# Performance work log

Measured on AMD Instinct MI355X. Metric: run time of the kernel, lower is better.

The kernel has to match this reference:

```python
import jax, jax.numpy as jnp
import numpy as np

H = 64  # base_hidden_size
SIGMA = 0.1
TAU = 1.0
T1 = 5
T2 = 5
NEG = 1e10


def setup_inputs() -> dict:
    key = jax.random.key(0)
    ks = jax.random.split(key, 24)
    B = 16
    R = 8
    n_cities = 1023
    n_nodes = n_cities + 1  # 1024

    x_a_state = jax.random.uniform(ks[0], (B, R, n_nodes), dtype=jnp.float32)
    assignment_prev = jnp.zeros((B, R, n_nodes), dtype=jnp.float32)
    # action: one-hot-ish; each robot picks a node. Use zeros + set robot r -> node r (valid: presence all ones)
    action = jnp.zeros((B, R, n_nodes), dtype=jnp.float32)
    action = action.at[:, jnp.arange(R), jnp.arange(R)].set(1.0)
    edge = jax.random.uniform(ks[1], (B, n_cities, n_nodes, 3), dtype=jnp.float32)
    avail_node_presence = jnp.ones((B, 1, n_nodes), dtype=jnp.float32)
    avail_robot = jnp.ones((B, 1, R), dtype=jnp.float32)

    def lin(k, i, o):
        # torch Linear weight [o, i]; store transposed [i, o]
        bound = 1.0 / np.sqrt(i)
        return jax.random.uniform(k, (i, o), dtype=jnp.float32, minval=-bound, maxval=bound)

    params = {
        'W1_presence': lin(ks[2], 3, H),
        'W2_presence': lin(ks[3], H, 1),
        'W_x_1a': lin(ks[4], 1, H),
        'W_emb_1a': lin(ks[5], 1, H),
        'W_l_1a': lin(ks[6], H, H),
        'W_x_1b': lin(ks[7], 1, H),
        'W_emb_1b': lin(ks[8], 1, H),
        'W_l_1b': lin(ks[9], H, H),
        'W_x_2': lin(ks[10], 2 * H, 2 * H),
        'W_emb_2': lin(ks[11], 1, 2 * H),
        'W_l_2': lin(ks[12], 2 * H, 2 * H),
        'W_Q': lin(ks[13], 2 * H, 1),
    }

    # noise initial states (randn in torch forward; make them explicit inputs for determinism)
    u_a0 = SIGMA * jax.random.normal(ks[14], (B, n_nodes, H), dtype=jnp.float32)
    u_b0 = SIGMA * jax.random.normal(ks[15], (B, n_nodes, H), dtype=jnp.float32)
    gamma0 = SIGMA * jax.random.normal(ks[16], (B, n_nodes, 2 * H), dtype=jnp.float32)

    return dict(x_a_state=x_a_state, assignment_prev=assignment_prev, action=action,
                edge=edge, avail_node_presence=avail_node_presence,
                u_a0=u_a0, u_b0=u_b0, gamma0=gamma0, **params)


def reference(x_a_state, assignment_prev, action, edge, avail_node_presence,
              u_a0, u_b0, gamma0,
              W1_presence, W2_presence, W_x_1a, W_emb_1a, W_l_1a,
              W_x_1b, W_emb_1b, W_l_1b, W_x_2, W_emb_2, W_l_2, W_Q):
    B, n_cities, n_nodes, _ = edge.shape

    assignment = assignment_prev + action  # [B,R,N]
    x_a = jnp.max(x_a_state * assignment, axis=1, keepdims=True)  # [B,1,N]
    x_a = jnp.transpose(x_a, (0, 2, 1))  # [B,N,1]

    # presence attention
    h1 = jax.nn.relu(edge @ W1_presence)          # [B,C,N,H]
    h2 = jax.nn.relu(h1 @ W2_presence)[..., 0]    # [B,C,N]
    h2 = h2 / TAU
    eye = jnp.eye(n_cities, n_nodes, dtype=edge.dtype)
    mask = (1.0 - eye)[None] * avail_node_presence  # [B,C,N]
    logit = h2 * mask - (1.0 - mask) * NEG
    presence_out = jax.nn.softmax(logit, axis=-1)   # [B,C,N]
    presence_in = jnp.transpose(presence_out, (0, 2, 1))  # [B,N,C]

    edge_dist = jnp.transpose(edge[:, :, :, 0:1], (0, 2, 1, 3))  # [B,N,C,1]

    # T1 loop (faithful to original incl. the l_a reuse in u_b update)
    emb_1a = jax.nn.sigmoid(edge_dist @ W_emb_1a)  # [B,N,C,H]
    emb_1b = jax.nn.sigmoid(edge_dist @ W_emb_1b)  # computed each iter but constant
    x_a_1a = x_a @ W_x_1a  # [B,N,H]
    x_a_1b = x_a @ W_x_1b

    u_a = u_a0
    for _ in range(T1):
        # u_a[:, :-1, :] gathered per target node i, weighted by emb and presence_in
        # l_a[b,i,h] = sum_c presence_in[b,i,c] * u_a[b,c,h] * emb_1a[b,i,c,h]
        l_a = jnp.einsum('bic,bch,bich->bih', presence_in, u_a[:, :-1, :], emb_1a)
        u_a = jax.nn.relu(l_a @ W_l_1a + x_a_1a)
        u_b = jax.nn.relu(l_a @ W_l_1b + x_a_1b)  # original uses l_a (bug kept)
    u_concat = jnp.concatenate([u_a, u_b], axis=-1)  # [B,N,2H]

    emb_2 = jax.nn.sigmoid(edge_dist @ W_emb_2)  # [B,N,C,2H]
    x2 = u_concat @ W_x_2  # [B,N,2H]
    gamma = gamma0
    for _ in range(T2):
        l_2 = jnp.einsum('bic,bch,bich->bih', presence_in, gamma[:, :-1, :], emb_2)
        gamma = jax.nn.relu(l_2 @ W_l_2 + x2)

    Q_utility = gamma @ W_Q  # [B,N,1]
    Q = jnp.sum(Q_utility, axis=1)  # [B,1]
    return Q
```

## Files before the change

kernel.cpp:

```cpp
#include <hip/hip_runtime.h>

#define BATCH 16
#define RB    8
#define CITIES 1023
#define NODES 1024
#define HDIM  64
#define H2DIM 128
#define KTOT  3072

#define C1f 0.24944119f
#define C3f (-0.01850586f)

typedef __bf16    bf16x8 __attribute__((ext_vector_type(8)));
typedef _Float16  f16x8  __attribute__((ext_vector_type(8)));
typedef _Float16  f16x2  __attribute__((ext_vector_type(2)));
typedef float     f32x4  __attribute__((ext_vector_type(4)));

__device__ __forceinline__ f32x4 mfma16(bf16x8 a, bf16x8 b, f32x4 c){
    return __builtin_amdgcn_mfma_f32_16x16x32_bf16(a, b, c, 0, 0, 0);
}
__device__ __forceinline__ f32x4 mfma16h(f16x8 a, f16x8 b, f32x4 c){
    return __builtin_amdgcn_mfma_f32_16x16x32_f16(a, b, c, 0, 0, 0);
}
__device__ __forceinline__ unsigned short f2b(float f){
    __bf16 b = (__bf16)f;
    return __builtin_bit_cast(unsigned short, b);
}
__device__ __forceinline__ float b2f(unsigned short u){
    unsigned int t = ((unsigned int)u) << 16;
    return __builtin_bit_cast(float, t);
}
__device__ __forceinline__ unsigned short f2h(float f){
    _Float16 h = (_Float16)f;
    return __builtin_bit_cast(unsigned short, h);
}
__device__ __forceinline__ float h2f(unsigned short u){
    return (float)__builtin_bit_cast(_Float16, u);
}
__device__ __forceinline__ void async16(const void* g, void* l){
    __builtin_amdgcn_global_load_lds(
        (const __attribute__((address_space(1))) unsigned int*)g,
        (__attribute__((address_space(3))) unsigned int*)l, 16, 0, 0);
}
template<int N>
__device__ __forceinline__ void wait_vmcnt(){
    asm volatile("s_waitcnt vmcnt(%0)" :: "i"(N) : "memory");
}

__global__ __launch_bounds__(256) void xa_k(const float* __restrict__ xs,
        const float* __restrict__ ap, const float* __restrict__ act,
        float* __restrict__ xa){
    int idx = blockIdx.x*256 + threadIdx.x;
    int b = idx >> 10, n = idx & 1023;
    float m = -1e30f;
    #pragma unroll
    for(int r=0;r<RB;r++){
        size_t o = (((size_t)b*RB + r)<<10) + n;
        m = fmaxf(m, xs[o]*(ap[o]+act[o]));
    }
    xa[idx] = m;
}

__global__ __launch_bounds__(128) void presence_k(const float* __restrict__ edge,
        const float* __restrict__ W1, const float* __restrict__ W2,
        const float* __restrict__ avail,
        unsigned short* __restrict__ P, unsigned short* __restrict__ D){
    int c = blockIdx.x, b = blockIdx.y;
    int tid = threadIdx.x;
    __shared__ f16x8 Wpk[32];
    __shared__ float red[2];
    if(tid < 32){
        int h0 = tid*2;
        f16x8 w;
        w[0]=(_Float16)W1[h0];       w[1]=(_Float16)W1[h0+1];
        w[2]=(_Float16)W1[64+h0];    w[3]=(_Float16)W1[64+h0+1];
        w[4]=(_Float16)W1[128+h0];   w[5]=(_Float16)W1[128+h0+1];
        w[6]=(_Float16)W2[h0];       w[7]=(_Float16)W2[h0+1];
        Wpk[tid] = w;
    }
    __syncthreads();
    f16x2 e0d[8], e1d[8], e2d[8];
    float acc[8];
    size_t ebase = (((size_t)b*CITIES + c)<<10)*3;
    #pragma unroll
    for(int j=0;j<8;j++){
        int n = tid + j*128;
        size_t ea = ebase + (size_t)n*3;
        _Float16 v0=(_Float16)edge[ea], v1=(_Float16)edge[ea+1], v2=(_Float16)edge[ea+2];
        e0d[j]=(f16x2){v0,v0}; e1d[j]=(f16x2){v1,v1}; e2d[j]=(f16x2){v2,v2};
        acc[j]=0.f;
    }
    const f16x2 z2 = {(_Float16)0, (_Float16)0};
    for(int hp=0;hp<32;hp++){
        f16x8 w = Wpk[hp];
        f16x2 wx={w[0],w[1]}, wy={w[2],w[3]}, wz={w[4],w[5]}, w2={w[6],w[7]};
        #pragma unroll
        for(int j=0;j<8;j++){
            f16x2 a = e0d[j]*wx + e1d[j]*wy + e2d[j]*wz;
            a = __builtin_elementwise_max(a, z2);
            acc[j] = __builtin_amdgcn_fdot2(a, w2, acc[j], false);
        }
    }
    float lg[8], ex[8];
    #pragma unroll
    for(int j=0;j<8;j++){
        int n = tid + j*128;
        float h2 = fmaxf(acc[j], 0.f);
        float mk = (n==c) ? 0.f : avail[(b<<10)+n];
        lg[j] = h2*mk - (1.f-mk)*1e10f;
    }
    int wv = tid>>6, ln = tid&63;
    float mx = -1e30f;
    #pragma unroll
    for(int j=0;j<8;j++) mx = fmaxf(mx, lg[j]);
    for(int o=32;o>0;o>>=1) mx = fmaxf(mx, __shfl_xor(mx,o,64));
    if(ln==0) red[wv]=mx;
    __syncthreads();
    mx = fmaxf(red[0],red[1]);
    __syncthreads();
    float s = 0.f;
    #pragma unroll
    for(int j=0;j<8;j++){ ex[j] = expf(lg[j]-mx); s += ex[j]; }
    for(int o=32;o>0;o>>=1) s += __shfl_xor(s,o,64);
    if(ln==0) red[wv]=s;
    __syncthreads();
    s = red[0]+red[1];
    float inv = 1.f/s;
    size_t pbase = ((size_t)b*CITIES + c)<<10;
    #pragma unroll
    for(int j=0;j<8;j++){
        int n = tid + j*128;
        P[pbase+n] = f2h(ex[j]*inv);
        D[pbase+n] = __builtin_bit_cast(unsigned short, e0d[j][0]);
    }
}

__global__ __launch_bounds__(256) void abuild_k(const unsigned short* __restrict__ P,
        const unsigned short* __restrict__ D, unsigned short* __restrict__ A){
    int ct = blockIdx.x, nt = blockIdx.y, b = blockIdx.z;
    int tid = threadIdx.x;
    __shared__ unsigned short Pt[32][36];
    __shared__ unsigned short Dt[32][36];
    {
        int crow = tid>>3, ng = (tid&7)<<2;
        int c = ct*32 + crow;
        if(c < CITIES){
            size_t o = (((size_t)b*CITIES + c)<<10) + nt*32 + ng;
            *(ushort4*)&Pt[crow][ng] = *(const ushort4*)&P[o];
            *(ushort4*)&Dt[crow][ng] = *(const ushort4*)&D[o];
        } else {
            ushort4 z; z.x=0;z.y=0;z.z=0;z.w=0;
            *(ushort4*)&Pt[crow][ng] = z;
            *(ushort4*)&Dt[crow][ng] = z;
        }
    }
    __syncthreads();
    int nrow = tid>>3, cg = (tid&7)<<2;
    ushort4 w0, w1, w2;
    #pragma unroll
    for(int j=0;j<4;j++){
        float p = h2f(Pt[cg+j][nrow]);
        float d = h2f(Dt[cg+j][nrow]);
        float d3 = d*d*d;
        ((unsigned short*)&w0)[j] = f2h(p);
        ((unsigned short*)&w1)[j] = f2h(p*d);
        ((unsigned short*)&w2)[j] = f2h(p*d3);
    }
    size_t abase = ((size_t)(b<<10) + nt*32 + nrow)*KTOT + ct*32 + cg;
    *(ushort4*)&A[abase]      = w0;
    *(ushort4*)&A[abase+1024] = w1;
    *(ushort4*)&A[abase+2048] = w2;
}

__global__ __launch_bounds__(256) void binit_k(const float* __restrict__ U0,
        const float* __restrict__ We, unsigned short* __restrict__ BT, int nout){
    int kc = blockIdx.x*256 + threadIdx.x;
    int h = blockIdx.y, b = blockIdx.z;
    int k = kc >> 10, c = kc & 1023;
    float we = We[h];
    float q = (k==0) ? 0.5f : (k==1 ? C1f*we : C3f*we*we*we);
    float u = (c < CITIES) ? U0[(((size_t)b<<10) + c)*nout + h] : 0.f;
    BT[((size_t)(b*nout + h))*KTOT + kc] = f2h(q*u);
}

#define SR 72

template<bool LAST>
__global__ __launch_bounds__(256) void fused1_k(const unsigned short* __restrict__ Ap,
        const unsigned short* __restrict__ BT,
        const float* __restrict__ Wl1a, const float* __restrict__ Wl1b,
        const float* __restrict__ Wx1a, const float* __restrict__ Wx1b,
        const float* __restrict__ We1a, const float* __restrict__ xa,
        unsigned short* __restrict__ Bnext, float* __restrict__ ua, float* __restrict__ ub){
    int mt = blockIdx.x, b = blockIdx.y;
    int i0 = mt*64;
    int tid = threadIdx.x, wave=tid>>6, lane=tid&63, quad=lane>>4, l16=lane&15;
    __shared__ __align__(16) char smem[49152];
    unsigned short* Lh = (unsigned short*)smem;
    unsigned short* Ll = (unsigned short*)(smem + 9216);
    unsigned short* Wh = (unsigned short*)(smem + 18432);
    unsigned short* Wo = (unsigned short*)(smem + 27648);

    f32x4 zero = {0.f,0.f,0.f,0.f};
    f32x4 gacc[4] = {zero,zero,zero,zero};
    const unsigned short* pa[2];
    const unsigned short* pb[2];
    #pragma unroll
    for(int rd=0; rd<2; rd++){
        int idx = rd*256 + tid, r = idx>>3, ch = idx&7;
        pa[rd] = Ap + ((size_t)(b<<10) + i0 + r)*KTOT + ((ch ^ (r&7))<<3);
        pb[rd] = BT + ((size_t)b*64 + r)*KTOT + ((ch ^ (r&7))<<3);
    }
    int sw = l16&7;
    auto stage = [&](char* buf){
        unsigned short* At = (unsigned short*)buf;
        unsigned short* Bt = At + 4096;
        #pragma unroll
        for(int rd=0; rd<2; rd++){ async16(pa[rd], At + rd*2048 + tid*8); pa[rd] += 64; }
        #pragma unroll
        for(int rd=0; rd<2; rd++){ async16(pb[rd], Bt + rd*2048 + tid*8); pb[rd] += 64; }
    };
    auto comp = [&](const char* buf){
        const unsigned short* At = (const unsigned short*)buf;
        const unsigned short* Bt = At + 4096;
        #pragma unroll
        for(int kb=0; kb<2; kb++){
            f16x8 af = *(const f16x8*)&At[(wave*16 + l16)*64 + (((kb*4+quad)^sw)<<3)];
            #pragma unroll
            for(int nt=0; nt<4; nt++){
                f16x8 bf = *(const f16x8*)&Bt[(nt*16 + l16)*64 + (((kb*4+quad)^sw)<<3)];
                gacc[nt] = mfma16h(af, bf, gacc[nt]);
            }
        }
    };
    char* b0 = smem; char* b1 = smem + 16384; char* b2 = smem + 32768;
    stage(b0); stage(b1);
    wait_vmcnt<4>(); __builtin_amdgcn_s_barrier();
    for(int kk=0; kk<46; kk++){
        stage(b2);
        comp(b0);
        wait_vmcnt<4>(); __builtin_amdgcn_s_barrier();
        char* tp=b0; b0=b1; b1=b2; b2=tp;
    }
    comp(b0);
    wait_vmcnt<0>(); __builtin_amdgcn_s_barrier();
    comp(b1);
    __syncthreads();
    #pragma unroll
    for(int nt=0; nt<4; nt++){
        int h = nt*16 + l16;
        #pragma unroll
        for(int rr=0; rr<4; rr++){
            int i = wave*16 + quad*4 + rr;
            float v = gacc[nt][rr];
            unsigned short hh = f2b(v);
            Lh[i*SR + h] = hh;
            Ll[i*SR + h] = f2b(v - b2f(hh));
        }
    }
    {
        int k = tid>>2, n0 = (tid&3)*16;
        for(int j=0;j<16;j++){
            float w = Wl1a[k*64 + n0 + j];
            unsigned short hh = f2b(w);
            Wh[(n0+j)*SR + k] = hh;
            Wo[(n0+j)*SR + k] = f2b(w - b2f(hh));
        }
    }
    __syncthreads();
    f32x4 acc[4] = {zero,zero,zero,zero};
    #pragma unroll
    for(int kc=0;kc<2;kc++){
        bf16x8 ah = *(const bf16x8*)&Lh[(wave*16+l16)*SR + kc*32 + quad*8];
        bf16x8 al = *(const bf16x8*)&Ll[(wave*16+l16)*SR + kc*32 + quad*8];
        #pragma unroll
        for(int nt=0;nt<4;nt++){
            bf16x8 bh = *(const bf16x8*)&Wh[(nt*16+l16)*SR + kc*32 + quad*8];
            bf16x8 bl = *(const bf16x8*)&Wo[(nt*16+l16)*SR + kc*32 + quad*8];
            acc[nt] = mfma16(ah, bh, acc[nt]);
            acc[nt] = mfma16(ah, bl, acc[nt]);
            acc[nt] = mfma16(al, bh, acc[nt]);
        }
    }
    int gi = i0 + wave*16 + quad*4;
    float4 xav = *(const float4*)&xa[(b<<10) + gi];
    float xr[4] = {xav.x, xav.y, xav.z, xav.w};
    if(!LAST){
        #pragma unroll
        for(int nt=0;nt<4;nt++){
            int h = nt*16 + l16;
            float wx = Wx1a[h];
            float we = We1a[h];
            float q1 = C1f*we, q2 = C3f*we*we*we;
            ushort4 w0,w1,w2;
            #pragma unroll
            for(int rr=0;rr<4;rr++){
                float u = fmaxf(acc[nt][rr] + xr[rr]*wx, 0.f);
                bool pad = (gi+rr == 1023);
                ((unsigned short*)&w0)[rr] = pad?(unsigned short)0:f2h(0.5f*u);
                ((unsigned short*)&w1)[rr] = pad?(unsigned short)0:f2h(q1*u);
                ((unsigned short*)&w2)[rr] = pad?(unsigned short)0:f2h(q2*u);
            }
            size_t base = ((size_t)(b*64 + h))*KTOT + gi;
            *(ushort4*)&Bnext[base]      = w0;
            *(ushort4*)&Bnext[base+1024] = w1;
            *(ushort4*)&Bnext[base+2048] = w2;
        }
    } else {
        #pragma unroll
        for(int nt=0;nt<4;nt++){
            int h = nt*16+l16; float wx = Wx1a[h];
            #pragma unroll
            for(int rr=0;rr<4;rr++)
                ua[(((size_t)b<<10)+gi+rr)*64 + h] = fmaxf(acc[nt][rr] + xr[rr]*wx, 0.f);
        }
        __syncthreads();
        { int k = tid>>2, n0 = (tid&3)*16;
          for(int j=0;j<16;j++){
              float w = Wl1b[k*64 + n0 + j];
              unsigned short hh = f2b(w);
              Wh[(n0+j)*SR + k] = hh;
              Wo[(n0+j)*SR + k] = f2b(w - b2f(hh));
          } }
        __syncthreads();
        f32x4 acc2[4] = {zero,zero,zero,zero};
        #pragma unroll
        for(int kc=0;kc<2;kc++){
            bf16x8 ah = *(const bf16x8*)&Lh[(wave*16+l16)*SR + kc*32 + quad*8];
            bf16x8 al = *(const bf16x8*)&Ll[(wave*16+l16)*SR + kc*32 + quad*8];
            #pragma unroll
            for(int nt=0;nt<4;nt++){
                bf16x8 bh = *(const bf16x8*)&Wh[(nt*16+l16)*SR + kc*32 + quad*8];
                bf16x8 bl = *(const bf16x8*)&Wo[(nt*16+l16)*SR + kc*32 + quad*8];
                acc2[nt] = mfma16(ah, bh, acc2[nt]);
                acc2[nt] = mfma16(ah, bl, acc2[nt]);
                acc2[nt] = mfma16(al, bh, acc2[nt]);
            }
        }
        #pragma unroll
        for(int nt=0;nt<4;nt++){
            int h = nt*16+l16; float wx = Wx1b[h];
            #pragma unroll
            for(int rr=0;rr<4;rr++)
                ub[(((size_t)b<<10)+gi+rr)*64 + h] = fmaxf(acc2[nt][rr] + xr[rr]*wx, 0.f);
        }
    }
}

__global__ __launch_bounds__(256) void x2_k(const float* __restrict__ ua,
        const float* __restrict__ ub, const float* __restrict__ Wx2,
        float* __restrict__ x2){
    int mt = blockIdx.x, b = blockIdx.y;
    int i0 = mt*64;
    int tid = threadIdx.x, wave=tid>>6, lane=tid&63, quad=lane>>4, l16=lane&15;
    __shared__ __align__(16) unsigned short Uh[64*SR], Ul[64*SR];
    __shared__ __align__(16) unsigned short Wh[128*SR], Wo[128*SR];
    f32x4 zero = {0.f,0.f,0.f,0.f};
    f32x4 acc[8];
    #pragma unroll
    for(int nt=0;nt<8;nt++) acc[nt]=zero;
    for(int ph=0; ph<2; ph++){
        if(ph) __syncthreads();
        {
            int k = tid>>2, n0 = (tid&3)*32;
            for(int j=0;j<32;j++){
                float w = Wx2[(ph*64 + k)*128 + n0 + j];
                unsigned short hh = f2b(w);
                Wh[(n0+j)*SR + k] = hh;
                Wo[(n0+j)*SR + k] = f2b(w - b2f(hh));
            }
            int i = tid>>2, c0 = (tid&3)*16;
            const float* src = (ph ? ub : ua) + (((size_t)b<<10)+i0+i)*64 + c0;
            #pragma unroll
            for(int j=0;j<4;j++){
                float4 v = *(const float4*)(src + j*4);
                float vv[4] = {v.x, v.y, v.z, v.w};
                #pragma unroll
                for(int t=0;t<4;t++){
                    unsigned short hh = f2b(vv[t]);
                    Uh[i*SR + c0 + j*4 + t] = hh;
                    Ul[i*SR + c0 + j*4 + t] = f2b(vv[t] - b2f(hh));
                }
            }
        }
        __syncthreads();
        #pragma unroll
        for(int kc=0;kc<2;kc++){
            bf16x8 ah = *(const bf16x8*)&Uh[(wave*16+l16)*SR + kc*32 + quad*8];
            bf16x8 al = *(const bf16x8*)&Ul[(wave*16+l16)*SR + kc*32 + quad*8];
            #pragma unroll
            for(int nt=0;nt<8;nt++){
                bf16x8 bh = *(const bf16x8*)&Wh[(nt*16+l16)*SR + kc*32 + quad*8];
                bf16x8 bl = *(const bf16x8*)&Wo[(nt*16+l16)*SR + kc*32 + quad*8];
                acc[nt] = mfma16(ah, bh, acc[nt]);
                acc[nt] = mfma16(ah, bl, acc[nt]);
                acc[nt] = mfma16(al, bh, acc[nt]);
            }
        }
    }
    int gi = i0 + wave*16 + quad*4;
    #pragma unroll
    for(int nt=0;nt<8;nt++){
        int h = nt*16 + l16;
        #pragma unroll
        for(int rr=0;rr<4;rr++)
            x2[(((size_t)b<<10)+gi+rr)*128 + h] = acc[nt][rr];
    }
}

template<bool LAST>
__global__ __launch_bounds__(256) void fused2_k(const unsigned short* __restrict__ Ap,
        const unsigned short* __restrict__ BT,
        const float* __restrict__ Wl2, const float* __restrict__ x2,
        const float* __restrict__ We2, const float* __restrict__ WQ,
        unsigned short* __restrict__ Bnext, float* __restrict__ out){
    int mt = blockIdx.x, b = blockIdx.y;
    int i0 = mt*64;
    int tid = threadIdx.x, wave=tid>>6, lane=tid&63, quad=lane>>4, l16=lane&15;
    extern __shared__ __align__(16) char smem[];
    __shared__ float red[4];
    unsigned short* Lh = (unsigned short*)smem;
    unsigned short* Ll = (unsigned short*)(smem + 9216);
    unsigned short* Wh = (unsigned short*)(smem + 18432);
    unsigned short* Wo = (unsigned short*)(smem + 36864);

    f32x4 zero = {0.f,0.f,0.f,0.f};
    f32x4 gacc[8] = {zero,zero,zero,zero,zero,zero,zero,zero};
    const unsigned short* pa[2];
    const unsigned short* pb[4];
    #pragma unroll
    for(int rd=0; rd<2; rd++){
        int idx = rd*256 + tid, r = idx>>3, ch = idx&7;
        pa[rd] = Ap + ((size_t)(b<<10) + i0 + r)*KTOT + ((ch ^ (r&7))<<3);
    }
    #pragma unroll
    for(int rd=0; rd<4; rd++){
        int idx = rd*256 + tid, r = idx>>3, ch = idx&7;
        pb[rd] = BT + ((size_t)b*128 + r)*KTOT + ((ch ^ (r&7))<<3);
    }
    int sw = l16&7;
    auto stage = [&](char* buf){
        unsigned short* At = (unsigned short*)buf;
        unsigned short* Bt = At + 4096;
        #pragma unroll
        for(int rd=0; rd<2; rd++){ async16(pa[rd], At + rd*2048 + tid*8); pa[rd] += 64; }
        #pragma unroll
        for(int rd=0; rd<4; rd++){ async16(pb[rd], Bt + rd*2048 + tid*8); pb[rd] += 64; }
    };
    auto comp = [&](const char* buf){
        const unsigned short* At = (const unsigned short*)buf;
        const unsigned short* Bt = At + 4096;
        #pragma unroll
        for(int kb=0; kb<2; kb++){
            f16x8 af = *(const f16x8*)&At[(wave*16 + l16)*64 + (((kb*4+quad)^sw)<<3)];
            #pragma unroll
            for(int nt=0; nt<8; nt++){
                f16x8 bf = *(const f16x8*)&Bt[(nt*16 + l16)*64 + (((kb*4+quad)^sw)<<3)];
                gacc[nt] = mfma16h(af, bf, gacc[nt]);
            }
        }
    };
    char* b0 = smem; char* b1 = smem + 24576; char* b2 = smem + 49152;
    stage(b0); stage(b1);
    wait_vmcnt<6>(); __builtin_amdgcn_s_barrier();
    for(int kk=0; kk<46; kk++){
        stage(b2);
        comp(b0);
        wait_vmcnt<6>(); __builtin_amdgcn_s_barrier();
        char* tp=b0; b0=b1; b1=b2; b2=tp;
    }
    comp(b0);
    wait_vmcnt<0>(); __builtin_amdgcn_s_barrier();
    comp(b1);
    __syncthreads();
    f32x4 fac[8] = {zero,zero,zero,zero,zero,zero,zero,zero};
    #pragma unroll
    for(int ph=0; ph<2; ph++){
        if(ph) __syncthreads();
        #pragma unroll
        for(int ntl=0; ntl<4; ntl++){
            int h = ntl*16 + l16;
            #pragma unroll
            for(int rr=0; rr<4; rr++){
                int i = wave*16 + quad*4 + rr;
                float v = gacc[ph*4 + ntl][rr];
                unsigned short hh = f2b(v);
                Lh[i*SR + h] = hh;
                Ll[i*SR + h] = f2b(v - b2f(hh));
            }
        }
        {
            int k = tid>>2, n0 = (tid&3)*32;
            for(int j=0;j<32;j++){
                float w = Wl2[(ph*64 + k)*128 + n0 + j];
                unsigned short hh = f2b(w);
                Wh[(n0+j)*SR + k] = hh;
                Wo[(n0+j)*SR + k] = f2b(w - b2f(hh));
            }
        }
        __syncthreads();
        #pragma unroll
        for(int kc=0;kc<2;kc++){
            bf16x8 ah = *(const bf16x8*)&Lh[(wave*16+l16)*SR + kc*32 + quad*8];
            bf16x8 al = *(const bf16x8*)&Ll[(wave*16+l16)*SR + kc*32 + quad*8];
            #pragma unroll
            for(int nt=0;nt<8;nt++){
                bf16x8 bh = *(const bf16x8*)&Wh[(nt*16+l16)*SR + kc*32 + quad*8];
                bf16x8 bl = *(const bf16x8*)&Wo[(nt*16+l16)*SR + kc*32 + quad*8];
                fac[nt] = mfma16(ah, bh, fac[nt]);
                fac[nt] = mfma16(ah, bl, fac[nt]);
                fac[nt] = mfma16(al, bh, fac[nt]);
            }
        }
    }
    int gi = i0 + wave*16 + quad*4;
    float qp = 0.f;
    #pragma unroll
    for(int nt=0;nt<8;nt++){
        int h = nt*16 + l16;
        float g[4];
        #pragma unroll
        for(int rr=0;rr<4;rr++)
            g[rr] = fmaxf(fac[nt][rr] + x2[(((size_t)b<<10)+gi+rr)*128 + h], 0.f);
        if(!LAST){
            float we = We2[h];
            float q1 = C1f*we, q2 = C3f*we*we*we;
            ushort4 w0,w1,w2;
            #pragma unroll
            for(int rr=0;rr<4;rr++){
                bool pad = (gi+rr == 1023);
                ((unsigned short*)&w0)[rr] = pad?(unsigned short)0:f2h(0.5f*g[rr]);
                ((unsigned short*)&w1)[rr] = pad?(unsigned short)0:f2h(q1*g[rr]);
                ((unsigned short*)&w2)[rr] = pad?(unsigned short)0:f2h(q2*g[rr]);
            }
            size_t base = ((size_t)(b*128 + h))*KTOT + gi;
            *(ushort4*)&Bnext[base]      = w0;
            *(ushort4*)&Bnext[base+1024] = w1;
            *(ushort4*)&Bnext[base+2048] = w2;
        } else {
            float wq = WQ[h];
            #pragma unroll
            for(int rr=0;rr<4;rr++) qp = fmaf(g[rr], wq, qp);
        }
    }
    if(LAST){
        for(int o=32;o>0;o>>=1) qp += __shfl_xor(qp,o,64);
        if(lane==0) red[wave]=qp;
        __syncthreads();
        if(tid==0) atomicAdd(&out[b], red[0]+red[1]+red[2]+red[3]);
    }
}

extern "C" void kernel_launch(void* const* d_in, const int* in_sizes, int n_in,
                              void* d_out, int out_size, void* d_ws, size_t ws_size,
                              hipStream_t stream){
    (void)in_sizes; (void)n_in; (void)out_size; (void)ws_size;
    const float* xs   = (const float*)d_in[0];
    const float* ap   = (const float*)d_in[1];
    const float* act  = (const float*)d_in[2];
    const float* edge = (const float*)d_in[3];
    const float* avail= (const float*)d_in[4];
    const float* ua0  = (const float*)d_in[5];
    const float* g0   = (const float*)d_in[7];
    const float* W1p  = (const float*)d_in[8];
    const float* W2p  = (const float*)d_in[9];
    const float* Wx1a = (const float*)d_in[10];
    const float* We1a = (const float*)d_in[11];
    const float* Wl1a = (const float*)d_in[12];
    const float* Wx1b = (const float*)d_in[13];
    const float* Wl1b = (const float*)d_in[15];
    const float* Wx2  = (const float*)d_in[16];
    const float* We2  = (const float*)d_in[17];
    const float* Wl2  = (const float*)d_in[18];
    const float* WQ   = (const float*)d_in[19];
    float* out = (float*)d_out;

    char* ws = (char*)d_ws;
    unsigned short* Abuf = (unsigned short*)ws;
    char* r2 = ws + 100663296;
    unsigned short* Pbuf = (unsigned short*)r2;
    unsigned short* Dbuf = (unsigned short*)(r2 + 33521664);
    unsigned short* BT1a = (unsigned short*)r2;
    unsigned short* BT1b = (unsigned short*)(r2 + 6291456);
    unsigned short* BT2a = (unsigned short*)(r2 + 12582912);
    unsigned short* BT2b = (unsigned short*)(r2 + 25165824);
    float* uaB           = (float*)(r2 + 117440512);
    float* ubB           = (float*)(r2 + 121634816);
    float* x2B           = (float*)(r2 + 125829120);
    float* xaB           = (float*)(r2 + 134217728);
    unsigned short* BT1[2] = {BT1a, BT1b};
    unsigned short* BT2[2] = {BT2a, BT2b};

    static bool attr_done = false;
    if(!attr_done){
        hipFuncSetAttribute((const void*)fused2_k<false>,
            hipFuncAttributeMaxDynamicSharedMemorySize, 73728);
        hipFuncSetAttribute((const void*)fused2_k<true>,
            hipFuncAttributeMaxDynamicSharedMemorySize, 73728);
        attr_done = true;
    }

    hipMemsetAsync(d_out, 0, BATCH*sizeof(float), stream);
    xa_k<<<64,256,0,stream>>>(xs, ap, act, xaB);
    presence_k<<<dim3(CITIES,BATCH),128,0,stream>>>(edge, W1p, W2p, avail, Pbuf, Dbuf);
    abuild_k<<<dim3(32,32,BATCH),256,0,stream>>>(Pbuf, Dbuf, Abuf);
    binit_k<<<dim3(12,64,BATCH),256,0,stream>>>(ua0, We1a, BT1[0], 64);
    for(int it=0; it<5; it++){
        if(it<4)
            fused1_k<false><<<dim3(16,16),256,0,stream>>>(Abuf, BT1[it&1], Wl1a, Wl1b,
                Wx1a, Wx1b, We1a, xaB, BT1[(it+1)&1], uaB, ubB);
        else
            fused1_k<true><<<dim3(16,16),256,0,stream>>>(Abuf, BT1[it&1], Wl1a, Wl1b,
                Wx1a, Wx1b, We1a, xaB, BT1[(it+1)&1], uaB, ubB);
    }
    x2_k<<<dim3(16,BATCH),256,0,stream>>>(uaB, ubB, Wx2, x2B);
    binit_k<<<dim3(12,128,BATCH),256,0,stream>>>(g0, We2, BT2[0], 128);
    for(int it=0; it<5; it++){
        if(it<4)
            fused2_k<false><<<dim3(16,16),256,73728,stream>>>(Abuf, BT2[it&1], Wl2, x2B,
                We2, WQ, BT2[(it+1)&1], out);
        else
            fused2_k<true><<<dim3(16,16),256,73728,stream>>>(Abuf, BT2[it&1], Wl2, x2B,
                We2, WQ, BT2[(it+1)&1], out);
    }
}
```

Measured before the change: 742.4 us.

## Halve row tile to 32 and split waves 2x2 to double grid size

Both fused propagation kernels now handle 32 target rows per block instead of 64. The four waves are arranged as 2 row-groups by 2 column-halves, and the grid doubles to 32x16 blocks. The aim is to fill more of the GPU's compute units (256 blocks was few for this device) and cut LDS per block, so occupancy improves. In exchange, each B tile is loaded from global memory twice as often, which raises L2/HBM traffic per unit of work, and each wave now runs fewer MFMAs per A fragment.

```diff
diff --git a/kernel.cpp b/kernel.cpp
--- a/kernel.cpp
+++ b/kernel.cpp
@@ -193,53 +193,56 @@
         const float* __restrict__ We1a, const float* __restrict__ xa,
         unsigned short* __restrict__ Bnext, float* __restrict__ ua, float* __restrict__ ub){
     int mt = blockIdx.x, b = blockIdx.y;
-    int i0 = mt*64;
+    int i0 = mt*32;
     int tid = threadIdx.x, wave=tid>>6, lane=tid&63, quad=lane>>4, l16=lane&15;
-    __shared__ __align__(16) char smem[49152];
+    int wm = wave>>1, wn = wave&1;
+    __shared__ __align__(16) char smem[36864];
     unsigned short* Lh = (unsigned short*)smem;
-    unsigned short* Ll = (unsigned short*)(smem + 9216);
-    unsigned short* Wh = (unsigned short*)(smem + 18432);
-    unsigned short* Wo = (unsigned short*)(smem + 27648);
+    unsigned short* Ll = (unsigned short*)(smem + 4608);
+    unsigned short* Wh = (unsigned short*)(smem + 9216);
+    unsigned short* Wo = (unsigned short*)(smem + 18432);
 
     f32x4 zero = {0.f,0.f,0.f,0.f};
-    f32x4 gacc[4] = {zero,zero,zero,zero};
-    const unsigned short* pa[2];
+    f32x4 gacc[2] = {zero,zero};
+    const unsigned short* pa;
     const unsigned short* pb[2];
+    {
+        int r = tid>>3, ch = tid&7;
+        pa = Ap + ((size_t)(b<<10) + i0 + r)*KTOT + ((ch ^ (r&7))<<3);
+    }
     #pragma unroll
     for(int rd=0; rd<2; rd++){
         int idx = rd*256 + tid, r = idx>>3, ch = idx&7;
-        pa[rd] = Ap + ((size_t)(b<<10) + i0 + r)*KTOT + ((ch ^ (r&7))<<3);
         pb[rd] = BT + ((size_t)b*64 + r)*KTOT + ((ch ^ (r&7))<<3);
     }
     int sw = l16&7;
     auto stage = [&](char* buf){
         unsigned short* At = (unsigned short*)buf;
-        unsigned short* Bt = At + 4096;
-        #pragma unroll
-        for(int rd=0; rd<2; rd++){ async16(pa[rd], At + rd*2048 + tid*8); pa[rd] += 64; }
+        unsigned short* Bt = At + 2048;
+        async16(pa, At + tid*8); pa += 64;
         #pragma unroll
         for(int rd=0; rd<2; rd++){ async16(pb[rd], Bt + rd*2048 + tid*8); pb[rd] += 64; }
     };
     auto comp = [&](const char* buf){
         const unsigned short* At = (const unsigned short*)buf;
-        const unsigned short* Bt = At + 4096;
+        const unsigned short* Bt = At + 2048;
         #pragma unroll
         for(int kb=0; kb<2; kb++){
-            f16x8 af = *(const f16x8*)&At[(wave*16 + l16)*64 + (((kb*4+quad)^sw)<<3)];
-            #pragma unroll
-            for(int nt=0; nt<4; nt++){
-                f16x8 bf = *(const f16x8*)&Bt[(nt*16 + l16)*64 + (((kb*4+quad)^sw)<<3)];
-                gacc[nt] = mfma16h(af, bf, gacc[nt]);
+            f16x8 af = *(const f16x8*)&At[(wm*16 + l16)*64 + (((kb*4+quad)^sw)<<3)];
+            #pragma unroll
+            for(int nt2=0; nt2<2; nt2++){
+                f16x8 bf = *(const f16x8*)&Bt[(wn*32 + nt2*16 + l16)*64 + (((kb*4+quad)^sw)<<3)];
+                gacc[nt2] = mfma16h(af, bf, gacc[nt2]);
             }
         }
     };
-    char* b0 = smem; char* b1 = smem + 16384; char* b2 = smem + 32768;
+    char* b0 = smem; char* b1 = smem + 12288; char* b2 = smem + 24576;
     stage(b0); stage(b1);
-    wait_vmcnt<4>(); __builtin_amdgcn_s_barrier();
+    wait_vmcnt<3>(); __builtin_amdgcn_s_barrier();
     for(int kk=0; kk<46; kk++){
         stage(b2);
         comp(b0);
-        wait_vmcnt<4>(); __builtin_amdgcn_s_barrier();
+        wait_vmcnt<3>(); __builtin_amdgcn_s_barrier();
         char* tp=b0; b0=b1; b1=b2; b2=tp;
     }
     comp(b0);
@@ -247,12 +250,12 @@
     comp(b1);
     __syncthreads();
     #pragma unroll
-    for(int nt=0; nt<4; nt++){
-        int h = nt*16 + l16;
+    for(int nt2=0; nt2<2; nt2++){
+        int h = wn*32 + nt2*16 + l16;
         #pragma unroll
         for(int rr=0; rr<4; rr++){
-            int i = wave*16 + quad*4 + rr;
-            float v = gacc[nt][rr];
+            int i = wm*16 + quad*4 + rr;
+            float v = gacc[nt2][rr];
             unsigned short hh = f2b(v);
             Lh[i*SR + h] = hh;
             Ll[i*SR + h] = f2b(v - b2f(hh));
@@ -268,34 +271,34 @@
         }
     }
     __syncthreads();
-    f32x4 acc[4] = {zero,zero,zero,zero};
+    f32x4 acc[2] = {zero,zero};
     #pragma unroll
     for(int kc=0;kc<2;kc++){
-        bf16x8 ah = *(const bf16x8*)&Lh[(wave*16+l16)*SR + kc*32 + quad*8];
-        bf16x8 al = *(const bf16x8*)&Ll[(wave*16+l16)*SR + kc*32 + quad*8];
-        #pragma unroll
-        for(int nt=0;nt<4;nt++){
-            bf16x8 bh = *(const bf16x8*)&Wh[(nt*16+l16)*SR + kc*32 + quad*8];
-            bf16x8 bl = *(const bf16x8*)&Wo[(nt*16+l16)*SR + kc*32 + quad*8];
-            acc[nt] = mfma16(ah, bh, acc[nt]);
-            acc[nt] = mfma16(ah, bl, acc[nt]);
-            acc[nt] = mfma16(al, bh, acc[nt]);
-        }
-    }
-    int gi = i0 + wave*16 + quad*4;
+        bf16x8 ah = *(const bf16x8*)&Lh[(wm*16+l16)*SR + kc*32 + quad*8];
+        bf16x8 al = *(const bf16x8*)&Ll[(wm*16+l16)*SR + kc*32 + quad*8];
+        #pragma unroll
+        for(int nt2=0;nt2<2;nt2++){
+            bf16x8 bh = *(const bf16x8*)&Wh[(wn*32+nt2*16+l16)*SR + kc*32 + quad*8];
+            bf16x8 bl = *(const bf16x8*)&Wo[(wn*32+nt2*16+l16)*SR + kc*32 + quad*8];
+            acc[nt2] = mfma16(ah, bh, acc[nt2]);
+            acc[nt2] = mfma16(ah, bl, acc[nt2]);
+            acc[nt2] = mfma16(al, bh, acc[nt2]);
+        }
+    }
+    int gi = i0 + wm*16 + quad*4;
     float4 xav = *(const float4*)&xa[(b<<10) + gi];
     float xr[4] = {xav.x, xav.y, xav.z, xav.w};
     if(!LAST){
         #pragma unroll
-        for(int nt=0;nt<4;nt++){
-            int h = nt*16 + l16;
+        for(int nt2=0;nt2<2;nt2++){
+            int h = wn*32 + nt2*16 + l16;
             float wx = Wx1a[h];
             float we = We1a[h];
             float q1 = C1f*we, q2 = C3f*we*we*we;
             ushort4 w0,w1,w2;
             #pragma unroll
             for(int rr=0;rr<4;rr++){
-                float u = fmaxf(acc[nt][rr] + xr[rr]*wx, 0.f);
+                float u = fmaxf(acc[nt2][rr] + xr[rr]*wx, 0.f);
                 bool pad = (gi+rr == 1023);
                 ((unsigned short*)&w0)[rr] = pad?(unsigned short)0:f2h(0.5f*u);
                 ((unsigned short*)&w1)[rr] = pad?(unsigned short)0:f2h(q1*u);
@@ -308,11 +311,11 @@
         }
     } else {
         #pragma unroll
-        for(int nt=0;nt<4;nt++){
-            int h = nt*16+l16; float wx = Wx1a[h];
+        for(int nt2=0;nt2<2;nt2++){
+            int h = wn*32 + nt2*16 + l16; float wx = Wx1a[h];
             #pragma unroll
             for(int rr=0;rr<4;rr++)
-                ua[(((size_t)b<<10)+gi+rr)*64 + h] = fmaxf(acc[nt][rr] + xr[rr]*wx, 0.f);
+                ua[(((size_t)b<<10)+gi+rr)*64 + h] = fmaxf(acc[nt2][rr] + xr[rr]*wx, 0.f);
         }
         __syncthreads();
         { int k = tid>>2, n0 = (tid&3)*16;
@@ -323,26 +326,26 @@
               Wo[(n0+j)*SR + k] = f2b(w - b2f(hh));
           } }
         __syncthreads();
-        f32x4 acc2[4] = {zero,zero,zero,zero};
+        f32x4 acc2[2] = {zero,zero};
         #pragma unroll
         for(int kc=0;kc<2;kc++){
-            bf16x8 ah = *(const bf16x8*)&Lh[(wave*16+l16)*SR + kc*32 + quad*8];
-            bf16x8 al = *(const bf16x8*)&Ll[(wave*16+l16)*SR + kc*32 + quad*8];
-            #pragma unroll
-            for(int nt=0;nt<4;nt++){
-                bf16x8 bh = *(const bf16x8*)&Wh[(nt*16+l16)*SR + kc*32 + quad*8];
-                bf16x8 bl = *(const bf16x8*)&Wo[(nt*16+l16)*SR + kc*32 + quad*8];
-                acc2[nt] = mfma16(ah, bh, acc2[nt]);
-                acc2[nt] = mfma16(ah, bl, acc2[nt]);
-                acc2[nt] = mfma16(al, bh, acc2[nt]);
-            }
-        }
-        #pragma unroll
-        for(int nt=0;nt<4;nt++){
-            int h = nt*16+l16; float wx = Wx1b[h];
+            bf16x8 ah = *(const bf16x8*)&Lh[(wm*16+l16)*SR + kc*32 + quad*8];
+            bf16x8 al = *(const bf16x8*)&Ll[(wm*16+l16)*SR + kc*32 + quad*8];
+            #pragma unroll
+            for(int nt2=0;nt2<2;nt2++){
+                bf16x8 bh = *(const bf16x8*)&Wh[(wn*32+nt2*16+l16)*SR + kc*32 + quad*8];
+                bf16x8 bl = *(const bf16x8*)&Wo[(wn*32+nt2*16+l16)*SR + kc*32 + quad*8];
+                acc2[nt2] = mfma16(ah, bh, acc2[nt2]);
+                acc2[nt2] = mfma16(ah, bl, acc2[nt2]);
+                acc2[nt2] = mfma16(al, bh, acc2[nt2]);
+            }
+        }
+        #pragma unroll
+        for(int nt2=0;nt2<2;nt2++){
+            int h = wn*32 + nt2*16 + l16; float wx = Wx1b[h];
             #pragma unroll
             for(int rr=0;rr<4;rr++)
-                ub[(((size_t)b<<10)+gi+rr)*64 + h] = fmaxf(acc2[nt][rr] + xr[rr]*wx, 0.f);
+                ub[(((size_t)b<<10)+gi+rr)*64 + h] = fmaxf(acc2[nt2][rr] + xr[rr]*wx, 0.f);
         }
     }
 }
@@ -415,23 +418,23 @@
         const float* __restrict__ We2, const float* __restrict__ WQ,
         unsigned short* __restrict__ Bnext, float* __restrict__ out){
     int mt = blockIdx.x, b = blockIdx.y;
-    int i0 = mt*64;
+    int i0 = mt*32;
     int tid = threadIdx.x, wave=tid>>6, lane=tid&63, quad=lane>>4, l16=lane&15;
-    extern __shared__ __align__(16) char smem[];
+    int wm = wave>>1, wn = wave&1;
+    __shared__ __align__(16) char smem[61440];
     __shared__ float red[4];
     unsigned short* Lh = (unsigned short*)smem;
-    unsigned short* Ll = (unsigned short*)(smem + 9216);
-    unsigned short* Wh = (unsigned short*)(smem + 18432);
-    unsigned short* Wo = (unsigned short*)(smem + 36864);
+    unsigned short* Ll = (unsigned short*)(smem + 4608);
+    unsigned short* Wh = (unsigned short*)(smem + 9216);
+    unsigned short* Wo = (unsigned short*)(smem + 27648);
 
     f32x4 zero = {0.f,0.f,0.f,0.f};
-    f32x4 gacc[8] = {zero,zero,zero,zero,zero,zero,zero,zero};
-    const unsigned short* pa[2];
+    f32x4 gacc[4] = {zero,zero,zero,zero};
+    const unsigned short* pa;
     const unsigned short* pb[4];
-    #pragma unroll
-    for(int rd=0; rd<2; rd++){
-        int idx = rd*256 + tid, r = idx>>3, ch = idx&7;
-        pa[rd] = Ap + ((size_t)(b<<10) + i0 + r)*KTOT + ((ch ^ (r&7))<<3);
+    {
+        int r = tid>>3, ch = tid&7;
+        pa = Ap + ((size_t)(b<<10) + i0 + r)*KTOT + ((ch ^ (r&7))<<3);
     }
     #pragma unroll
     for(int rd=0; rd<4; rd++){
@@ -441,52 +444,53 @@
     int sw = l16&7;
     auto stage = [&](char* buf){
         unsigned short* At = (unsigned short*)buf;
-        unsigned short* Bt = At + 4096;
-        #pragma unroll
-        for(int rd=0; rd<2; rd++){ async16(pa[rd], At + rd*2048 + tid*8); pa[rd] += 64; }
+        unsigned short* Bt = At + 2048;
+        async16(pa, At + tid*8); pa += 64;
         #pragma unroll
         for(int rd=0; rd<4; rd++){ async16(pb[rd], Bt + rd*2048 + tid*8); pb[rd] += 64; }
     };
     auto comp = [&](const char* buf){
         const unsigned short* At = (const unsigned short*)buf;
-        const unsigned short* Bt = At + 4096;
+        const unsigned short* Bt = At + 2048;
         #pragma unroll
         for(int kb=0; kb<2; kb++){
-            f16x8 af = *(const f16x8*)&At[(wave*16 + l16)*64 + (((kb*4+quad)^sw)<<3)];
-            #pragma unroll
-            for(int nt=0; nt<8; nt++){
-                f16x8 bf = *(const f16x8*)&Bt[(nt*16 + l16)*64 + (((kb*4+quad)^sw)<<3)];
+            f16x8 af = *(const f16x8*)&At[(wm*16 + l16)*64 + (((kb*4+quad)^sw)<<3)];
+            #pragma unroll
+            for(int nt=0; nt<4; nt++){
+                f16x8 bf = *(const f16x8*)&Bt[(wn*64 + nt*16 + l16)*64 + (((kb*4+quad)^sw)<<3)];
                 gacc[nt] = mfma16h(af, bf, gacc[nt]);
             }
         }
     };
-    char* b0 = smem; char* b1 = smem + 24576; char* b2 = smem + 49152;
+    char* b0 = smem; char* b1 = smem + 20480; char* b2 = smem + 40960;
     stage(b0); stage(b1);
-    wait_vmcnt<6>(); __builtin_amdgcn_s_barrier();
+    wait_vmcnt<5>(); __builtin_amdgcn_s_barrier();
     for(int kk=0; kk<46; kk++){
         stage(b2);
         comp(b0);
-        wait_vmcnt<6>(); __builtin_amdgcn_s_barrier();
+        wait_vmcnt<5>(); __builtin_amdgcn_s_barrier();
         char* tp=b0; b0=b1; b1=b2; b2=tp;
     }
     comp(b0);
     wait_vmcnt<0>(); __builtin_amdgcn_s_barrier();
     comp(b1);
     __syncthreads();
-    f32x4 fac[8] = {zero,zero,zero,zero,zero,zero,zero,zero};
+    f32x4 fac[4] = {zero,zero,zero,zero};
     #pragma unroll
     for(int ph=0; ph<2; ph++){
         if(ph) __syncthreads();
-        #pragma unroll
-        for(int ntl=0; ntl<4; ntl++){
-            int h = ntl*16 + l16;
-            #pragma unroll
-            for(int rr=0; rr<4; rr++){
-                int i = wave*16 + quad*4 + rr;
-                float v = gacc[ph*4 + ntl][rr];
-                unsigned short hh = f2b(v);
-                Lh[i*SR + h] = hh;
-                Ll[i*SR + h] = f2b(v - b2f(hh));
+        if(wn == ph){
+            #pragma unroll
+            for(int nt=0; nt<4; nt++){
+                int hh_col = nt*16 + l16;
+                #pragma unroll
+                for(int rr=0; rr<4; rr++){
+                    int i = wm*16 + quad*4 + rr;
+                    float v = gacc[nt][rr];
+                    unsigned short hh = f2b(v);
+                    Lh[i*SR + hh_col] = hh;
+                    Ll[i*SR + hh_col] = f2b(v - b2f(hh));
+                }
             }
         }
         {
@@ -501,23 +505,23 @@
         __syncthreads();
         #pragma unroll
         for(int kc=0;kc<2;kc++){
-            bf16x8 ah = *(const bf16x8*)&Lh[(wave*16+l16)*SR + kc*32 + quad*8];
-            bf16x8 al = *(const bf16x8*)&Ll[(wave*16+l16)*SR + kc*32 + quad*8];
-            #pragma unroll
-            for(int nt=0;nt<8;nt++){
-                bf16x8 bh = *(const bf16x8*)&Wh[(nt*16+l16)*SR + kc*32 + quad*8];
-                bf16x8 bl = *(const bf16x8*)&Wo[(nt*16+l16)*SR + kc*32 + quad*8];
+            bf16x8 ah = *(const bf16x8*)&Lh[(wm*16+l16)*SR + kc*32 + quad*8];
+            bf16x8 al = *(const bf16x8*)&Ll[(wm*16+l16)*SR + kc*32 + quad*8];
+            #pragma unroll
+            for(int nt=0;nt<4;nt++){
+                bf16x8 bh = *(const bf16x8*)&Wh[(wn*64+nt*16+l16)*SR + kc*32 + quad*8];
+                bf16x8 bl = *(const bf16x8*)&Wo[(wn*64+nt*16+l16)*SR + kc*32 + quad*8];
                 fac[nt] = mfma16(ah, bh, fac[nt]);
                 fac[nt] = mfma16(ah, bl, fac[nt]);
                 fac[nt] = mfma16(al, bh, fac[nt]);
             }
         }
     }
-    int gi = i0 + wave*16 + quad*4;
+    int gi = i0 + wm*16 + quad*4;
     float qp = 0.f;
     #pragma unroll
-    for(int nt=0;nt<8;nt++){
-        int h = nt*16 + l16;
+    for(int nt=0;nt<4;nt++){
+        int h = wn*64 + nt*16 + l16;
         float g[4];
         #pragma unroll
         for(int rr=0;rr<4;rr++)
@@ -591,15 +595,6 @@
     unsigned short* BT1[2] = {BT1a, BT1b};
     unsigned short* BT2[2] = {BT2a, BT2b};
 
-    static bool attr_done = false;
-    if(!attr_done){
-        hipFuncSetAttribute((const void*)fused2_k<false>,
-            hipFuncAttributeMaxDynamicSharedMemorySize, 73728);
-        hipFuncSetAttribute((const void*)fused2_k<true>,
-            hipFuncAttributeMaxDynamicSharedMemorySize, 73728);
-        attr_done = true;
-    }
-
     hipMemsetAsync(d_out, 0, BATCH*sizeof(float), stream);
     xa_k<<<64,256,0,stream>>>(xs, ap, act, xaB);
     presence_k<<<dim3(CITIES,BATCH),128,0,stream>>>(edge, W1p, W2p, avail, Pbuf, Dbuf);
@@ -607,20 +602,20 @@
     binit_k<<<dim3(12,64,BATCH),256,0,stream>>>(ua0, We1a, BT1[0], 64);
     for(int it=0; it<5; it++){
         if(it<4)
-            fused1_k<false><<<dim3(16,16),256,0,stream>>>(Abuf, BT1[it&1], Wl1a, Wl1b,
+            fused1_k<false><<<dim3(32,16),256,0,stream>>>(Abuf, BT1[it&1], Wl1a, Wl1b,
                 Wx1a, Wx1b, We1a, xaB, BT1[(it+1)&1], uaB, ubB);
         else
-            fused1_k<true><<<dim3(16,16),256,0,stream>>>(Abuf, BT1[it&1], Wl1a, Wl1b,
+            fused1_k<true><<<dim3(32,16),256,0,stream>>>(Abuf, BT1[it&1], Wl1a, Wl1b,
                 Wx1a, Wx1b, We1a, xaB, BT1[(it+1)&1], uaB, ubB);
     }
     x2_k<<<dim3(16,BATCH),256,0,stream>>>(uaB, ubB, Wx2, x2B);
     binit_k<<<dim3(12,128,BATCH),256,0,stream>>>(g0, We2, BT2[0], 128);
     for(int it=0; it<5; it++){
         if(it<4)
-            fused2_k<false><<<dim3(16,16),256,73728,stream>>>(Abuf, BT2[it&1], Wl2, x2B,
+            fused2_k<false><<<dim3(32,16),256,0,stream>>>(Abuf, BT2[it&1], Wl2, x2B,
                 We2, WQ, BT2[(it+1)&1], out);
         else
-            fused2_k<true><<<dim3(16,16),256,73728,stream>>>(Abuf, BT2[it&1], Wl2, x2B,
+            fused2_k<true><<<dim3(32,16),256,0,stream>>>(Abuf, BT2[it&1], Wl2, x2B,
                 We2, WQ, BT2[(it+1)&1], out);
     }
 }
```

Measured after the change: 744.3 us. Within noise of the previous version (+0.2%).
